# Kernel tuning notes

Measured on AMD Instinct MI355X. Metric: run time of the kernel, lower is better.

## Reference

```python
import jax, jax.numpy as jnp
import numpy as np
import math

N = 400000  # total anchors across FPN levels
M = 128     # GT boxes per image
IOU_LOW, IOU_HIGH = 0.3, 0.6
SCALE_CLAMP = math.log(224.0 / 8.0)
NEUTRAL = -1.0e8


def setup_inputs() -> dict:
    key = jax.random.key(0)
    k1, k2, k3, k4, k5, k6 = jax.random.split(key, 6)
    # anchors: valid XYXY boxes centered in an 800x800 image
    ctr = jax.random.uniform(k1, (N, 2), minval=0.0, maxval=800.0)
    half = jax.random.uniform(k2, (N, 2), minval=8.0, maxval=64.0)
    anchors = jnp.concatenate([ctr - half, ctr + half], axis=1)
    deltas = jax.random.normal(k3, (N, 4)) * 0.2
    # GT boxes (M, 5): XYXY + class id
    gctr = jax.random.uniform(k4, (M, 2), minval=0.0, maxval=800.0)
    ghalf = jax.random.uniform(k5, (M, 2), minval=10.0, maxval=120.0)
    cls = jnp.floor(jax.random.uniform(k6, (M, 1), minval=0.0, maxval=20.0))
    gt_boxes = jnp.concatenate([gctr - ghalf, gctr + ghalf, cls], axis=1)
    return {"anchors": anchors, "deltas": deltas, "gt_boxes": gt_boxes}


def apply_deltas_to_anchors(deltas, anchors):
    # mirrors rcnn_apply_deltas_to_anchors (note: pw/ph are HALF widths/heights)
    dx = deltas[:, 0]
    dy = deltas[:, 1]
    dw = jnp.minimum(deltas[:, 2], SCALE_CLAMP)
    dh = jnp.minimum(deltas[:, 3], SCALE_CLAMP)
    px = (anchors[:, 0] + anchors[:, 2]) * 0.5
    py = (anchors[:, 1] + anchors[:, 3]) * 0.5
    pw = (anchors[:, 2] - anchors[:, 0]) * 0.5
    ph = (anchors[:, 3] - anchors[:, 1]) * 0.5
    bx = px + pw * dx
    by = py + ph * dy
    bw = pw * jnp.exp(dw)
    bh = ph * jnp.exp(dh)
    return jnp.stack([bx - bw, by - bh, bx + bw, by + bh], axis=-1)


def pairwise_iou(b1, b2):
    # (Nm, 4) x (Nn, 4) -> (Nm, Nn), XYXY format, mirrors iou()
    x1 = jnp.maximum(b1[:, None, 0], b2[None, :, 0])
    y1 = jnp.maximum(b1[:, None, 1], b2[None, :, 1])
    x2 = jnp.minimum(b1[:, None, 2], b2[None, :, 2])
    y2 = jnp.minimum(b1[:, None, 3], b2[None, :, 3])
    xl = x2 - x1
    yl = y2 - y1
    inter = jnp.where((xl > 0) & (yl > 0), xl * yl, 0.0)
    area1 = (b1[:, 2] - b1[:, 0]) * (b1[:, 3] - b1[:, 1])
    area2 = (b2[:, 2] - b2[:, 0]) * (b2[:, 3] - b2[:, 1])
    union = area1[:, None] + area2[None, :] - inter
    return inter / union


def reference(anchors, deltas, gt_boxes):
    proposals = apply_deltas_to_anchors(deltas, anchors)
    # 2) match anchors to GT (rcnn_match_anchors_to_gt).
    #    Invalid GT (class == -1) are masked out of the IoU matrix instead of
    #    filtered (keeps static shapes under jit).
    valid = gt_boxes[:, 4] != -1
    m = pairwise_iou(anchors, gt_boxes[:, :4])          # (N, M)
    m = jnp.where(valid[None, :], m, -1.0)
    match_quality = jnp.max(m, axis=1)                   # (N,)
    matched_idxs = jnp.argmax(m, axis=1)                 # (N,)
    matched_gt = gt_boxes[matched_idxs]                  # (N, 5)
    matched_gt = jnp.where((match_quality <= IOU_LOW)[:, None], -1.0, matched_gt)
    neutral = (match_quality > IOU_LOW) & (match_quality < IOU_HIGH)
    matched_gt = jnp.where(neutral[:, None], NEUTRAL, matched_gt)
    return proposals, matched_gt
```

## Files before the change

kernel.cpp:

```cpp
#include <hip/hip_runtime.h>
#include <math.h>

#define MAX_GT 128

__global__ __launch_bounds__(256) void rpn_match_kernel(
    const float* __restrict__ anchors,
    const float* __restrict__ deltas,
    const float* __restrict__ gt_boxes,
    float* __restrict__ out,
    int n, int m)
{
    __shared__ float sx0[MAX_GT], sy0[MAX_GT], sx1[MAX_GT], sy1[MAX_GT];
    __shared__ float sarea[MAX_GT], smask[MAX_GT];
    __shared__ float sg[MAX_GT][5];

    const int tid = threadIdx.x;
    if (tid < m) {
        float g0 = gt_boxes[tid * 5 + 0];
        float g1 = gt_boxes[tid * 5 + 1];
        float g2 = gt_boxes[tid * 5 + 2];
        float g3 = gt_boxes[tid * 5 + 3];
        float g4 = gt_boxes[tid * 5 + 4];
        sx0[tid] = g0; sy0[tid] = g1; sx1[tid] = g2; sy1[tid] = g3;
        sarea[tid] = (g2 - g0) * (g3 - g1);
        smask[tid] = (g4 != -1.0f) ? 1.0f : 0.0f;
        sg[tid][0] = g0; sg[tid][1] = g1; sg[tid][2] = g2;
        sg[tid][3] = g3; sg[tid][4] = g4;
    }
    __syncthreads();

    const int i = blockIdx.x * 256 + tid;
    if (i >= n) return;

    const float4 a = reinterpret_cast<const float4*>(anchors)[i];
    const float4 d = reinterpret_cast<const float4*>(deltas)[i];

    const float SCALE_CLAMP = 3.3322045101752038f;
    float dx = d.x;
    float dy = d.y;
    float dw = fminf(d.z, SCALE_CLAMP);
    float dh = fminf(d.w, SCALE_CLAMP);
    float px = (a.x + a.z) * 0.5f;
    float py = (a.y + a.w) * 0.5f;
    float pw = (a.z - a.x) * 0.5f;
    float ph = (a.w - a.y) * 0.5f;
    float bx = px + pw * dx;
    float by = py + ph * dy;
    float bw = pw * expf(dw);
    float bh = ph * expf(dh);
    float4 prop;
    prop.x = bx - bw;
    prop.y = by - bh;
    prop.z = bx + bw;
    prop.w = by + bh;
    reinterpret_cast<float4*>(out)[i] = prop;

    const float area1 = (a.z - a.x) * (a.w - a.y);

    float best = -3.0f;
    int bidx = 0;
    #pragma unroll 4
    for (int j = 0; j < m; ++j) {
        float x1 = fmaxf(a.x, sx0[j]);
        float y1 = fmaxf(a.y, sy0[j]);
        float x2 = fminf(a.z, sx1[j]);
        float y2 = fminf(a.w, sy1[j]);
        float xl = x2 - x1;
        float yl = y2 - y1;
        float inter = ((xl > 0.0f) && (yl > 0.0f)) ? (xl * yl) : 0.0f;
        float uni = (area1 + sarea[j]) - inter;
        float iou = inter / uni;
        iou = (smask[j] != 0.0f) ? iou : -1.0f;
        if (iou > best) { best = iou; bidx = j; }
    }

    const float IOU_LOW = 0.3f, IOU_HIGH = 0.6f, NEUTRAL = -100000000.0f;
    float o0, o1, o2, o3, o4;
    if (best <= IOU_LOW) {
        o0 = o1 = o2 = o3 = o4 = -1.0f;
    } else if (best < IOU_HIGH) {
        o0 = o1 = o2 = o3 = o4 = NEUTRAL;
    } else {
        o0 = sg[bidx][0]; o1 = sg[bidx][1]; o2 = sg[bidx][2];
        o3 = sg[bidx][3]; o4 = sg[bidx][4];
    }
    float* mo = out + (size_t)n * 4 + (size_t)i * 5;
    mo[0] = o0; mo[1] = o1; mo[2] = o2; mo[3] = o3; mo[4] = o4;
}

extern "C" void kernel_launch(void* const* d_in, const int* in_sizes, int n_in,
                              void* d_out, int out_size, void* d_ws, size_t ws_size,
                              hipStream_t stream) {
    const float* anchors  = (const float*)d_in[0];
    const float* deltas   = (const float*)d_in[1];
    const float* gt_boxes = (const float*)d_in[2];
    float* out = (float*)d_out;

    int n = in_sizes[0] / 4;
    int m = in_sizes[2] / 5;

    int nblocks = (n + 255) / 256;
    hipLaunchKernelGGL(rpn_match_kernel, dim3(nblocks), dim3(256), 0, stream,
                       anchors, deltas, gt_boxes, out, n, m);
}
```

Baseline: 112.2 us.

## Drop per-pair IoU division via cross-multiplied compare and process two anchors per thread

Removes the per-pair floating divide in the IoU argmax by tracking the best intersection and area-sum and comparing candidates through cross-multiplication, dividing only once at the end. Invalid GT boxes are turned into degenerate boxes with zero area in shared memory, so the mask check leaves the inner loop. GT boxes are packed as float4 for a single LDS read per box. Each thread now handles two anchors so each shared-memory load is reused twice, at the cost of more registers and half as many blocks. Tie-breaking and edge cases such as all-zero intersections or all-invalid GTs may differ slightly from the original comparison semantics.

```diff
diff --git a/kernel.cpp b/kernel.cpp
--- a/kernel.cpp
+++ b/kernel.cpp
@@ -10,9 +10,9 @@
     float* __restrict__ out,
     int n, int m)
 {
-    __shared__ float sx0[MAX_GT], sy0[MAX_GT], sx1[MAX_GT], sy1[MAX_GT];
-    __shared__ float sarea[MAX_GT], smask[MAX_GT];
-    __shared__ float sg[MAX_GT][5];
+    __shared__ float4 sbox[MAX_GT];
+    __shared__ float  sarea[MAX_GT];
+    __shared__ float  scls[MAX_GT];
 
     const int tid = threadIdx.x;
     if (tid < m) {
@@ -21,71 +21,127 @@
         float g2 = gt_boxes[tid * 5 + 2];
         float g3 = gt_boxes[tid * 5 + 3];
         float g4 = gt_boxes[tid * 5 + 4];
-        sx0[tid] = g0; sy0[tid] = g1; sx1[tid] = g2; sy1[tid] = g3;
-        sarea[tid] = (g2 - g0) * (g3 - g1);
-        smask[tid] = (g4 != -1.0f) ? 1.0f : 0.0f;
-        sg[tid][0] = g0; sg[tid][1] = g1; sg[tid][2] = g2;
-        sg[tid][3] = g3; sg[tid][4] = g4;
+        bool valid = (g4 != -1.0f);
+        sbox[tid] = valid ? make_float4(g0, g1, g2, g3)
+                          : make_float4(1e30f, 1e30f, -1e30f, -1e30f);
+        sarea[tid] = valid ? (g2 - g0) * (g3 - g1) : 0.0f;
+        scls[tid]  = g4;
     }
     __syncthreads();
 
-    const int i = blockIdx.x * 256 + tid;
-    if (i >= n) return;
+    const int i0 = blockIdx.x * 512 + tid;
+    const int i1 = i0 + 256;
+    const bool v0 = (i0 < n);
+    const bool v1 = (i1 < n);
+    const int i0c = v0 ? i0 : 0;
+    const int i1c = v1 ? i1 : 0;
 
-    const float4 a = reinterpret_cast<const float4*>(anchors)[i];
-    const float4 d = reinterpret_cast<const float4*>(deltas)[i];
+    const float4 a0 = reinterpret_cast<const float4*>(anchors)[i0c];
+    const float4 a1 = reinterpret_cast<const float4*>(anchors)[i1c];
+    const float4 d0 = reinterpret_cast<const float4*>(deltas)[i0c];
+    const float4 d1 = reinterpret_cast<const float4*>(deltas)[i1c];
 
     const float SCALE_CLAMP = 3.3322045101752038f;
-    float dx = d.x;
-    float dy = d.y;
-    float dw = fminf(d.z, SCALE_CLAMP);
-    float dh = fminf(d.w, SCALE_CLAMP);
-    float px = (a.x + a.z) * 0.5f;
-    float py = (a.y + a.w) * 0.5f;
-    float pw = (a.z - a.x) * 0.5f;
-    float ph = (a.w - a.y) * 0.5f;
-    float bx = px + pw * dx;
-    float by = py + ph * dy;
-    float bw = pw * expf(dw);
-    float bh = ph * expf(dh);
-    float4 prop;
-    prop.x = bx - bw;
-    prop.y = by - bh;
-    prop.z = bx + bw;
-    prop.w = by + bh;
-    reinterpret_cast<float4*>(out)[i] = prop;
+    {
+        float pw = (a0.z - a0.x) * 0.5f, ph = (a0.w - a0.y) * 0.5f;
+        float px = (a0.x + a0.z) * 0.5f, py = (a0.y + a0.w) * 0.5f;
+        float bx = px + pw * d0.x, by = py + ph * d0.y;
+        float bw = pw * expf(fminf(d0.z, SCALE_CLAMP));
+        float bh = ph * expf(fminf(d0.w, SCALE_CLAMP));
+        if (v0) reinterpret_cast<float4*>(out)[i0] =
+            make_float4(bx - bw, by - bh, bx + bw, by + bh);
+    }
+    {
+        float pw = (a1.z - a1.x) * 0.5f, ph = (a1.w - a1.y) * 0.5f;
+        float px = (a1.x + a1.z) * 0.5f, py = (a1.y + a1.w) * 0.5f;
+        float bx = px + pw * d1.x, by = py + ph * d1.y;
+        float bw = pw * expf(fminf(d1.z, SCALE_CLAMP));
+        float bh = ph * expf(fminf(d1.w, SCALE_CLAMP));
+        if (v1) reinterpret_cast<float4*>(out)[i1] =
+            make_float4(bx - bw, by - bh, bx + bw, by + bh);
+    }
 
-    const float area1 = (a.z - a.x) * (a.w - a.y);
+    const float ar0 = (a0.z - a0.x) * (a0.w - a0.y);
+    const float ar1 = (a1.z - a1.x) * (a1.w - a1.y);
 
-    float best = -3.0f;
-    int bidx = 0;
-    #pragma unroll 4
-    for (int j = 0; j < m; ++j) {
-        float x1 = fmaxf(a.x, sx0[j]);
-        float y1 = fmaxf(a.y, sy0[j]);
-        float x2 = fminf(a.z, sx1[j]);
-        float y2 = fminf(a.w, sy1[j]);
-        float xl = x2 - x1;
-        float yl = y2 - y1;
-        float inter = ((xl > 0.0f) && (yl > 0.0f)) ? (xl * yl) : 0.0f;
-        float uni = (area1 + sarea[j]) - inter;
-        float iou = inter / uni;
-        iou = (smask[j] != 0.0f) ? iou : -1.0f;
-        if (iou > best) { best = iou; bidx = j; }
+    float4 b = sbox[0];
+    float ga = sarea[0];
+    float bI0, bS0, bI1, bS1;
+    int bidx0 = 0, bidx1 = 0;
+    {
+        float xl = fminf(a0.z, b.z) - fmaxf(a0.x, b.x);
+        float yl = fminf(a0.w, b.w) - fmaxf(a0.y, b.y);
+        bI0 = fmaxf(xl, 0.0f) * fmaxf(yl, 0.0f);
+        bS0 = ar0 + ga;
+        xl = fminf(a1.z, b.z) - fmaxf(a1.x, b.x);
+        yl = fminf(a1.w, b.w) - fmaxf(a1.y, b.y);
+        bI1 = fmaxf(xl, 0.0f) * fmaxf(yl, 0.0f);
+        bS1 = ar1 + ga;
+    }
+
+    #pragma unroll 8
+    for (int j = 1; j < m; ++j) {
+        b  = sbox[j];
+        ga = sarea[j];
+        {
+            float xl = fminf(a0.z, b.z) - fmaxf(a0.x, b.x);
+            float yl = fminf(a0.w, b.w) - fmaxf(a0.y, b.y);
+            float inter = fmaxf(xl, 0.0f) * fmaxf(yl, 0.0f);
+            float S = ar0 + ga;
+            bool g = (inter * bS0) > (bI0 * S);
+            bI0   = g ? inter : bI0;
+            bS0   = g ? S     : bS0;
+            bidx0 = g ? j     : bidx0;
+        }
+        {
+            float xl = fminf(a1.z, b.z) - fmaxf(a1.x, b.x);
+            float yl = fminf(a1.w, b.w) - fmaxf(a1.y, b.y);
+            float inter = fmaxf(xl, 0.0f) * fmaxf(yl, 0.0f);
+            float S = ar1 + ga;
+            bool g = (inter * bS1) > (bI1 * S);
+            bI1   = g ? inter : bI1;
+            bS1   = g ? S     : bS1;
+            bidx1 = g ? j     : bidx1;
+        }
     }
 
     const float IOU_LOW = 0.3f, IOU_HIGH = 0.6f, NEUTRAL = -100000000.0f;
-    float o0, o1, o2, o3, o4;
-    if (best <= IOU_LOW) {
-        o0 = o1 = o2 = o3 = o4 = -1.0f;
-    } else if (best < IOU_HIGH) {
-        o0 = o1 = o2 = o3 = o4 = NEUTRAL;
-    } else {
-        o0 = sg[bidx][0]; o1 = sg[bidx][1]; o2 = sg[bidx][2];
-        o3 = sg[bidx][3]; o4 = sg[bidx][4];
+    float* mout = out + (size_t)n * 4;
+
+    {
+        float uni = bS0 - bI0;
+        float q = bI0 / uni;
+        float o0, o1, o2, o3, o4;
+        if (q <= IOU_LOW) {
+            o0 = o1 = o2 = o3 = o4 = -1.0f;
+        } else if (q < IOU_HIGH) {
+            o0 = o1 = o2 = o3 = o4 = NEUTRAL;
+        } else {
+            float4 gbx = sbox[bidx0];
+            o0 = gbx.x; o1 = gbx.y; o2 = gbx.z; o3 = gbx.w; o4 = scls[bidx0];
+        }
+        if (v0) {
+            float* mo = mout + (size_t)i0 * 5;
+            mo[0] = o0; mo[1] = o1; mo[2] = o2; mo[3] = o3; mo[4] = o4;
+        }
     }
-    float* mo = out + (size_t)n * 4 + (size_t)i * 5;
-    mo[0] = o0; mo[1] = o1; mo[2] = o2; mo[3] = o3; mo[4] = o4;
+    {
+        float uni = bS1 - bI1;
+        float q = bI1 / uni;
+        float o0, o1, o2, o3, o4;
+        if (q <= IOU_LOW) {
+            o0 = o1 = o2 = o3 = o4 = -1.0f;
+        } else if (q < IOU_HIGH) {
+            o0 = o1 = o2 = o3 = o4 = NEUTRAL;
+        } else {
+            float4 gbx = sbox[bidx1];
+            o0 = gbx.x; o1 = gbx.y; o2 = gbx.z; o3 = gbx.w; o4 = scls[bidx1];
+        }
+        if (v1) {
+            float* mo = mout + (size_t)i1 * 5;
+            mo[0] = o0; mo[1] = o1; mo[2] = o2; mo[3] = o3; mo[4] = o4;
+        }
+    }
 }
 
 extern "C" void kernel_launch(void* const* d_in, const int* in_sizes, int n_in,
@@ -99,7 +155,7 @@
     int n = in_sizes[0] / 4;
     int m = in_sizes[2] / 5;
 
-    int nblocks = (n + 255) / 256;
+    int nblocks = (n + 511) / 512;
     hipLaunchKernelGGL(rpn_match_kernel, dim3(nblocks), dim3(256), 0, stream,
                        anchors, deltas, gt_boxes, out, n, m);
 }
```

Result: faster. 94.36 us (-15.9%).

## Process four anchors per thread with division-free IoU argmax and packed math

Applied to the files above, without the earlier changes.

Each thread now handles four anchors, and the GT table is read straight from global/scalar memory instead of being staged in LDS. The per-pair division is replaced by cross-multiplied comparison of inter/sum ratios, with one division per anchor at the end. Two anchors are packed into float2 vectors to allow packed FP32 ops. This cuts divide cost and LDS traffic per pair, but raises register pressure and relies on the cross-multiply comparison matching argmax tie behaviour and rounding.

```diff
diff --git a/kernel.cpp b/kernel.cpp
--- a/kernel.cpp
+++ b/kernel.cpp
@@ -1,91 +1,129 @@
 #include <hip/hip_runtime.h>
 #include <math.h>
 
-#define MAX_GT 128
+typedef float v2f __attribute__((ext_vector_type(2)));
 
-__global__ __launch_bounds__(256) void rpn_match_kernel(
+static __device__ __forceinline__ v2f v2_min(v2f a, float b) {
+    v2f r; r.x = fminf(a.x, b); r.y = fminf(a.y, b); return r;
+}
+static __device__ __forceinline__ v2f v2_max(v2f a, float b) {
+    v2f r; r.x = fmaxf(a.x, b); r.y = fmaxf(a.y, b); return r;
+}
+static __device__ __forceinline__ v2f v2_max0(v2f a) {
+    v2f r; r.x = fmaxf(a.x, 0.0f); r.y = fmaxf(a.y, 0.0f); return r;
+}
+
+__global__ __launch_bounds__(128) void rpn_match_kernel(
     const float* __restrict__ anchors,
     const float* __restrict__ deltas,
     const float* __restrict__ gt_boxes,
     float* __restrict__ out,
     int n, int m)
 {
-    __shared__ float sx0[MAX_GT], sy0[MAX_GT], sx1[MAX_GT], sy1[MAX_GT];
-    __shared__ float sarea[MAX_GT], smask[MAX_GT];
-    __shared__ float sg[MAX_GT][5];
+    const int tid = threadIdx.x;
+    const int base = blockIdx.x * 512 + tid;
 
-    const int tid = threadIdx.x;
-    if (tid < m) {
-        float g0 = gt_boxes[tid * 5 + 0];
-        float g1 = gt_boxes[tid * 5 + 1];
-        float g2 = gt_boxes[tid * 5 + 2];
-        float g3 = gt_boxes[tid * 5 + 3];
-        float g4 = gt_boxes[tid * 5 + 4];
-        sx0[tid] = g0; sy0[tid] = g1; sx1[tid] = g2; sy1[tid] = g3;
-        sarea[tid] = (g2 - g0) * (g3 - g1);
-        smask[tid] = (g4 != -1.0f) ? 1.0f : 0.0f;
-        sg[tid][0] = g0; sg[tid][1] = g1; sg[tid][2] = g2;
-        sg[tid][3] = g3; sg[tid][4] = g4;
+    int  idx[4];
+    bool vld[4];
+    float4 a[4], d[4];
+    #pragma unroll
+    for (int k = 0; k < 4; ++k) {
+        int i = base + 128 * k;
+        vld[k] = (i < n);
+        idx[k] = vld[k] ? i : 0;
     }
-    __syncthreads();
-
-    const int i = blockIdx.x * 256 + tid;
-    if (i >= n) return;
-
-    const float4 a = reinterpret_cast<const float4*>(anchors)[i];
-    const float4 d = reinterpret_cast<const float4*>(deltas)[i];
+    #pragma unroll
+    for (int k = 0; k < 4; ++k) {
+        a[k] = reinterpret_cast<const float4*>(anchors)[idx[k]];
+        d[k] = reinterpret_cast<const float4*>(deltas)[idx[k]];
+    }
 
     const float SCALE_CLAMP = 3.3322045101752038f;
-    float dx = d.x;
-    float dy = d.y;
-    float dw = fminf(d.z, SCALE_CLAMP);
-    float dh = fminf(d.w, SCALE_CLAMP);
-    float px = (a.x + a.z) * 0.5f;
-    float py = (a.y + a.w) * 0.5f;
-    float pw = (a.z - a.x) * 0.5f;
-    float ph = (a.w - a.y) * 0.5f;
-    float bx = px + pw * dx;
-    float by = py + ph * dy;
-    float bw = pw * expf(dw);
-    float bh = ph * expf(dh);
-    float4 prop;
-    prop.x = bx - bw;
-    prop.y = by - bh;
-    prop.z = bx + bw;
-    prop.w = by + bh;
-    reinterpret_cast<float4*>(out)[i] = prop;
-
-    const float area1 = (a.z - a.x) * (a.w - a.y);
-
-    float best = -3.0f;
-    int bidx = 0;
-    #pragma unroll 4
-    for (int j = 0; j < m; ++j) {
-        float x1 = fmaxf(a.x, sx0[j]);
-        float y1 = fmaxf(a.y, sy0[j]);
-        float x2 = fminf(a.z, sx1[j]);
-        float y2 = fminf(a.w, sy1[j]);
-        float xl = x2 - x1;
-        float yl = y2 - y1;
-        float inter = ((xl > 0.0f) && (yl > 0.0f)) ? (xl * yl) : 0.0f;
-        float uni = (area1 + sarea[j]) - inter;
-        float iou = inter / uni;
-        iou = (smask[j] != 0.0f) ? iou : -1.0f;
-        if (iou > best) { best = iou; bidx = j; }
+    #pragma unroll
+    for (int k = 0; k < 4; ++k) {
+        float pw = (a[k].z - a[k].x) * 0.5f, ph = (a[k].w - a[k].y) * 0.5f;
+        float px = (a[k].x + a[k].z) * 0.5f, py = (a[k].y + a[k].w) * 0.5f;
+        float bx = px + pw * d[k].x, by = py + ph * d[k].y;
+        float bw = pw * expf(fminf(d[k].z, SCALE_CLAMP));
+        float bh = ph * expf(fminf(d[k].w, SCALE_CLAMP));
+        if (vld[k]) reinterpret_cast<float4*>(out)[idx[k]] =
+            make_float4(bx - bw, by - bh, bx + bw, by + bh);
     }
 
-    const float IOU_LOW = 0.3f, IOU_HIGH = 0.6f, NEUTRAL = -100000000.0f;
-    float o0, o1, o2, o3, o4;
-    if (best <= IOU_LOW) {
-        o0 = o1 = o2 = o3 = o4 = -1.0f;
-    } else if (best < IOU_HIGH) {
-        o0 = o1 = o2 = o3 = o4 = NEUTRAL;
-    } else {
-        o0 = sg[bidx][0]; o1 = sg[bidx][1]; o2 = sg[bidx][2];
-        o3 = sg[bidx][3]; o4 = sg[bidx][4];
+    {
+        #pragma clang fp contract(off)
+        v2f ax[2], ay[2], az[2], aw[2], ar[2], bI[2], bS[2];
+        int bidx[4];
+        #pragma unroll
+        for (int p = 0; p < 2; ++p) {
+            ax[p].x = a[2*p].x;   ax[p].y = a[2*p+1].x;
+            ay[p].x = a[2*p].y;   ay[p].y = a[2*p+1].y;
+            az[p].x = a[2*p].z;   az[p].y = a[2*p+1].z;
+            aw[p].x = a[2*p].w;   aw[p].y = a[2*p+1].w;
+            ar[p].x = (a[2*p].z   - a[2*p].x)   * (a[2*p].w   - a[2*p].y);
+            ar[p].y = (a[2*p+1].z - a[2*p+1].x) * (a[2*p+1].w - a[2*p+1].y);
+            bI[p].x = -1.0f; bI[p].y = -1.0f;
+            bS[p].x =  1.0f; bS[p].y =  1.0f;
+        }
+        bidx[0] = bidx[1] = bidx[2] = bidx[3] = 0;
+
+        #pragma unroll 8
+        for (int j = 0; j < m; ++j) {
+            float g0 = gt_boxes[j * 5 + 0];
+            float g1 = gt_boxes[j * 5 + 1];
+            float g2 = gt_boxes[j * 5 + 2];
+            float g3 = gt_boxes[j * 5 + 3];
+            float g4 = gt_boxes[j * 5 + 4];
+            bool valid = (g4 != -1.0f);
+            g0 = valid ? g0 : 0.0f;
+            g1 = valid ? g1 : 0.0f;
+            g2 = valid ? g2 : 0.0f;
+            g3 = valid ? g3 : 0.0f;
+            float ga = (g2 - g0) * (g3 - g1);
+
+            #pragma unroll
+            for (int p = 0; p < 2; ++p) {
+                v2f xl = v2_min(az[p], g2) - v2_max(ax[p], g0);
+                v2f yl = v2_min(aw[p], g3) - v2_max(ay[p], g1);
+                v2f inter = v2_max0(xl) * v2_max0(yl);
+                v2f S = ar[p] + ga;
+                v2f lhs = inter * bS[p];
+                v2f rhs = bI[p] * S;
+                bool w0 = lhs.x > rhs.x;
+                bool w1 = lhs.y > rhs.y;
+                bI[p].x   = w0 ? inter.x : bI[p].x;
+                bS[p].x   = w0 ? S.x     : bS[p].x;
+                bidx[2*p] = w0 ? j       : bidx[2*p];
+                bI[p].y     = w1 ? inter.y : bI[p].y;
+                bS[p].y     = w1 ? S.y     : bS[p].y;
+                bidx[2*p+1] = w1 ? j       : bidx[2*p+1];
+            }
+        }
+
+        const float IOU_LOW = 0.3f, IOU_HIGH = 0.6f, NEUTRAL = -100000000.0f;
+        float* mout = out + (size_t)n * 4;
+
+        #pragma unroll
+        for (int k = 0; k < 4; ++k) {
+            float I = (k & 1) ? bI[k >> 1].y : bI[k >> 1].x;
+            float S = (k & 1) ? bS[k >> 1].y : bS[k >> 1].x;
+            float uni = S - I;
+            float q = I / uni;
+            float o0, o1, o2, o3, o4;
+            if (q <= IOU_LOW) {
+                o0 = o1 = o2 = o3 = o4 = -1.0f;
+            } else if (q < IOU_HIGH) {
+                o0 = o1 = o2 = o3 = o4 = NEUTRAL;
+            } else {
+                const float* row = gt_boxes + (size_t)bidx[k] * 5;
+                o0 = row[0]; o1 = row[1]; o2 = row[2]; o3 = row[3]; o4 = row[4];
+            }
+            if (vld[k]) {
+                float* mo = mout + (size_t)idx[k] * 5;
+                mo[0] = o0; mo[1] = o1; mo[2] = o2; mo[3] = o3; mo[4] = o4;
+            }
+        }
     }
-    float* mo = out + (size_t)n * 4 + (size_t)i * 5;
-    mo[0] = o0; mo[1] = o1; mo[2] = o2; mo[3] = o3; mo[4] = o4;
 }
 
 extern "C" void kernel_launch(void* const* d_in, const int* in_sizes, int n_in,
@@ -99,7 +137,7 @@
     int n = in_sizes[0] / 4;
     int m = in_sizes[2] / 5;
 
-    int nblocks = (n + 255) / 256;
-    hipLaunchKernelGGL(rpn_match_kernel, dim3(nblocks), dim3(256), 0, stream,
+    int nblocks = (n + 511) / 512;
+    hipLaunchKernelGGL(rpn_match_kernel, dim3(nblocks), dim3(128), 0, stream,
                        anchors, deltas, gt_boxes, out, n, m);
 }
```

Result: faster. 102.7 us (-8.5%).

## Replace per-GT IoU division with cross-multiplied comparison and read GT boxes directly

Applied to the files above, without the earlier changes.

The argmax loop no longer divides per GT. It compares candidates by cross-multiplying intersection against area sum (inter/(S-inter) is monotonic in inter/S), and does a single division at the end. The shared-memory staging and __syncthreads are removed, and GT boxes are read from global memory (uniform, likely scalar/cached loads). Invalid GTs are masked by an infinite area. This removes the per-iteration divide and the block barrier, at the cost of possible differences in tie-breaking and rounding compared with the reference IoU ordering.

```diff
diff --git a/kernel.cpp b/kernel.cpp
--- a/kernel.cpp
+++ b/kernel.cpp
@@ -1,7 +1,5 @@
 #include <hip/hip_runtime.h>
 #include <math.h>
-
-#define MAX_GT 128
 
 __global__ __launch_bounds__(256) void rpn_match_kernel(
     const float* __restrict__ anchors,
@@ -10,82 +8,69 @@
     float* __restrict__ out,
     int n, int m)
 {
-    __shared__ float sx0[MAX_GT], sy0[MAX_GT], sx1[MAX_GT], sy1[MAX_GT];
-    __shared__ float sarea[MAX_GT], smask[MAX_GT];
-    __shared__ float sg[MAX_GT][5];
-
-    const int tid = threadIdx.x;
-    if (tid < m) {
-        float g0 = gt_boxes[tid * 5 + 0];
-        float g1 = gt_boxes[tid * 5 + 1];
-        float g2 = gt_boxes[tid * 5 + 2];
-        float g3 = gt_boxes[tid * 5 + 3];
-        float g4 = gt_boxes[tid * 5 + 4];
-        sx0[tid] = g0; sy0[tid] = g1; sx1[tid] = g2; sy1[tid] = g3;
-        sarea[tid] = (g2 - g0) * (g3 - g1);
-        smask[tid] = (g4 != -1.0f) ? 1.0f : 0.0f;
-        sg[tid][0] = g0; sg[tid][1] = g1; sg[tid][2] = g2;
-        sg[tid][3] = g3; sg[tid][4] = g4;
-    }
-    __syncthreads();
-
-    const int i = blockIdx.x * 256 + tid;
+    const int i = blockIdx.x * 256 + threadIdx.x;
     if (i >= n) return;
 
     const float4 a = reinterpret_cast<const float4*>(anchors)[i];
     const float4 d = reinterpret_cast<const float4*>(deltas)[i];
 
     const float SCALE_CLAMP = 3.3322045101752038f;
-    float dx = d.x;
-    float dy = d.y;
-    float dw = fminf(d.z, SCALE_CLAMP);
-    float dh = fminf(d.w, SCALE_CLAMP);
-    float px = (a.x + a.z) * 0.5f;
-    float py = (a.y + a.w) * 0.5f;
-    float pw = (a.z - a.x) * 0.5f;
-    float ph = (a.w - a.y) * 0.5f;
-    float bx = px + pw * dx;
-    float by = py + ph * dy;
-    float bw = pw * expf(dw);
-    float bh = ph * expf(dh);
-    float4 prop;
-    prop.x = bx - bw;
-    prop.y = by - bh;
-    prop.z = bx + bw;
-    prop.w = by + bh;
-    reinterpret_cast<float4*>(out)[i] = prop;
-
-    const float area1 = (a.z - a.x) * (a.w - a.y);
-
-    float best = -3.0f;
-    int bidx = 0;
-    #pragma unroll 4
-    for (int j = 0; j < m; ++j) {
-        float x1 = fmaxf(a.x, sx0[j]);
-        float y1 = fmaxf(a.y, sy0[j]);
-        float x2 = fminf(a.z, sx1[j]);
-        float y2 = fminf(a.w, sy1[j]);
-        float xl = x2 - x1;
-        float yl = y2 - y1;
-        float inter = ((xl > 0.0f) && (yl > 0.0f)) ? (xl * yl) : 0.0f;
-        float uni = (area1 + sarea[j]) - inter;
-        float iou = inter / uni;
-        iou = (smask[j] != 0.0f) ? iou : -1.0f;
-        if (iou > best) { best = iou; bidx = j; }
+    {
+        float pw = (a.z - a.x) * 0.5f, ph = (a.w - a.y) * 0.5f;
+        float px = (a.x + a.z) * 0.5f, py = (a.y + a.w) * 0.5f;
+        float bx = px + pw * d.x, by = py + ph * d.y;
+        float bw = pw * expf(fminf(d.z, SCALE_CLAMP));
+        float bh = ph * expf(fminf(d.w, SCALE_CLAMP));
+        reinterpret_cast<float4*>(out)[i] =
+            make_float4(bx - bw, by - bh, bx + bw, by + bh);
     }
 
-    const float IOU_LOW = 0.3f, IOU_HIGH = 0.6f, NEUTRAL = -100000000.0f;
-    float o0, o1, o2, o3, o4;
-    if (best <= IOU_LOW) {
-        o0 = o1 = o2 = o3 = o4 = -1.0f;
-    } else if (best < IOU_HIGH) {
-        o0 = o1 = o2 = o3 = o4 = NEUTRAL;
-    } else {
-        o0 = sg[bidx][0]; o1 = sg[bidx][1]; o2 = sg[bidx][2];
-        o3 = sg[bidx][3]; o4 = sg[bidx][4];
+    {
+        #pragma clang fp contract(off)
+        const float ar = (a.z - a.x) * (a.w - a.y);
+
+        float bI = -1.0f, bS = 1.0f;
+        int bidx = 0;
+
+        #pragma unroll 8
+        for (int j = 0; j < m; ++j) {
+            float g0 = gt_boxes[j * 5 + 0];
+            float g1 = gt_boxes[j * 5 + 1];
+            float g2 = gt_boxes[j * 5 + 2];
+            float g3 = gt_boxes[j * 5 + 3];
+            float g4 = gt_boxes[j * 5 + 4];
+            float ga = (g2 - g0) * (g3 - g1);
+            ga = (g4 != -1.0f) ? ga : __builtin_inff();
+
+            float x1 = fmaxf(a.x, g0);
+            float y1 = fmaxf(a.y, g1);
+            float x2 = fminf(a.z, g2);
+            float y2 = fminf(a.w, g3);
+            float xl = x2 - x1;
+            float yl = y2 - y1;
+            float inter = fmaxf(xl, 0.0f) * fmaxf(yl, 0.0f);
+            float S = ar + ga;
+            bool w = (inter * bS) > (bI * S);
+            bI   = w ? inter : bI;
+            bS   = w ? S     : bS;
+            bidx = w ? j     : bidx;
+        }
+
+        const float IOU_LOW = 0.3f, IOU_HIGH = 0.6f, NEUTRAL = -100000000.0f;
+        float uni = bS - bI;
+        float q = bI / uni;
+        float o0, o1, o2, o3, o4;
+        if (q <= IOU_LOW) {
+            o0 = o1 = o2 = o3 = o4 = -1.0f;
+        } else if (q < IOU_HIGH) {
+            o0 = o1 = o2 = o3 = o4 = NEUTRAL;
+        } else {
+            const float* row = gt_boxes + (size_t)bidx * 5;
+            o0 = row[0]; o1 = row[1]; o2 = row[2]; o3 = row[3]; o4 = row[4];
+        }
+        float* mo = out + (size_t)n * 4 + (size_t)i * 5;
+        mo[0] = o0; mo[1] = o1; mo[2] = o2; mo[3] = o3; mo[4] = o4;
     }
-    float* mo = out + (size_t)n * 4 + (size_t)i * 5;
-    mo[0] = o0; mo[1] = o1; mo[2] = o2; mo[3] = o3; mo[4] = o4;
 }
 
 extern "C" void kernel_launch(void* const* d_in, const int* in_sizes, int n_in,
```

Measured after the change: 100.9 us. -10.1%, faster.
